# Kernel tuning notes

Measured on AMD Instinct MI355X. Metric: run time of the kernel, lower is better.

## Reference

```python
import jax, jax.numpy as jnp
import numpy as np

# --- dims (match init_kwargs) ---
B, T, S, K = 4, 128, 64, 2
CS = 1024            # codebook_size
NOTE_V, PHON_V = 128, 64
NE, PE, SE, PGB, PGE = 128, 128, 16, 8, 32
COND, TOK, PREV, D = 256, 256, 256, 512
NH, L_CTX, L_AUD = 8, 4, 6
HIST_WIN, AUD_WIN = 32, 64
DFF = 4 * D

CTX_KEYS = ["ln1_w","ln1_b","in_w","in_b","out_w","out_b","ln2_w","ln2_b","f1_w","f1_b","f2_w","f2_b"]


def _ln(x, w, b):
    m = x.mean(-1, keepdims=True)
    v = ((x - m) ** 2).mean(-1, keepdims=True)
    return (x - m) / jnp.sqrt(v + 1e-5) * w + b


def _mlp2(x, w1, b1, w2, b2, act):
    return act(x @ w1.T + b1) @ w2.T + b2


def _local_mask(n, win):
    i = jnp.arange(n)
    d = i[:, None] - i[None, :]
    return (d < 0) | (d >= win)   # True = masked (causal, local window)


def _mha(x, mask, in_w, in_b, out_w, out_b, nh):
    b, s, d = x.shape
    dh = d // nh
    q, k, v = jnp.split(x @ in_w.T + in_b, 3, axis=-1)
    sp = lambda t: t.reshape(b, s, nh, dh).transpose(0, 2, 1, 3)
    q, k, v = sp(q), sp(k), sp(v)
    sc = jnp.einsum('bhqd,bhkd->bhqk', q, k) * (1.0 / np.sqrt(dh))
    sc = jnp.where(mask, -1e9, sc)
    a = jax.nn.softmax(sc, axis=-1)
    o = jnp.einsum('bhqk,bhkd->bhqd', a, v).transpose(0, 2, 1, 3).reshape(b, s, d)
    return o @ out_w.T + out_b


def _block(x, mask, pr, nh):
    # pr: dict with ln1_w..f2_b for one layer (pre-norm attn + FFN, GELU)
    h = _ln(x, pr["ln1_w"], pr["ln1_b"])
    x = x + _mha(h, mask, pr["in_w"], pr["in_b"], pr["out_w"], pr["out_b"], nh)
    h2 = _ln(x, pr["ln2_w"], pr["ln2_b"])
    return x + _mlp2(h2, pr["f1_w"], pr["f1_b"], pr["f2_w"], pr["f2_b"],
                     lambda z: jax.nn.gelu(z, approximate=False))


def _forward(p, codes, note_id, phoneme_id, slur, phone_progress):
    silu = jax.nn.silu
    # ---- condition encoder ----
    cond_in = jnp.concatenate([
        p["note_emb_w"][note_id], p["phoneme_emb_w"][phoneme_id],
        p["slur_emb_w"][jnp.clip(slur, 0, 1)], p["pp_emb_w"][phone_progress]], -1)
    cond = _mlp2(cond_in, p["cond_w1"], p["cond_b1"], p["cond_w2"], p["cond_b2"], silu)
    # ---- shifted prev-step representation ----
    first = codes[..., 0]                       # [B,T,S]
    pooled = p["token_emb_w"][first].mean(2)    # [B,T,TOK]
    prev = _mlp2(pooled, p["prev_w1"], p["prev_b1"], p["prev_w2"], p["prev_b2"], silu)
    bos = jnp.broadcast_to(p["bos_step"], (B, 1, PREV))
    prev = jnp.concatenate([bos, prev[:, :-1]], 1)
    # ---- context transformer over steps (local causal window) ----
    h = _mlp2(jnp.concatenate([cond, prev], -1), p["step_w1"], p["step_b1"], p["step_w2"], p["step_b2"], silu)
    m_ctx = _local_mask(T, HIST_WIN)
    for l in range(L_CTX):
        pr = {k: p["ctx_" + k][l] for k in CTX_KEYS}
        h = _block(h, m_ctx, pr, NH)
    # ---- audio decoder over frames within each step ----
    tok = p["token_emb_w"][first] @ p["audio_in_w"].T + p["audio_in_b"]   # [B,T,S,D]
    bos_a = jnp.broadcast_to(p["audio_bos"], (B, T, 1, D))
    a = jnp.concatenate([bos_a, tok[:, :, :-1]], 2) + p["frame_pos"][None, None] + h[:, :, None]
    a = a.reshape(B * T, S, D)
    m_a = _local_mask(S, min(AUD_WIN, S))
    for l in range(L_AUD):
        pr = {k: p["aud_" + k][l] for k in CTX_KEYS}
        a = _block(a, m_a, pr, NH)
    ah = a.reshape(B, T, S, D)
    # ---- heads ----
    first_logits = (ah @ p["first_w"].T + p["first_b"])[..., None, :]     # [B,T,S,1,CS]
    rh = _mlp2(jnp.concatenate([ah, tok], -1), p["resc_w1"], p["resc_b1"], p["resc_w2"], p["resc_b2"], silu)
    res = jnp.einsum('btsd,kcd->btskc', rh, p["res_w"]) + p["res_b"]       # [B,T,S,K-1,CS]
    return jnp.concatenate([first_logits, res], axis=3)                    # [B,T,S,K,CS]


def setup_inputs() -> dict:
    key = jax.random.key(0)
    ks = iter(jax.random.split(key, 128))
    w = lambda *sh: jax.random.normal(next(ks), sh, jnp.float32) * 0.02
    z = lambda *sh: jnp.zeros(sh, jnp.float32)
    o = lambda *sh: jnp.ones(sh, jnp.float32)
    inp = {
        "codes": jax.random.randint(next(ks), (B, T, S, K), 0, CS, jnp.int32),
        "note_id": jax.random.randint(next(ks), (B, T), 0, NOTE_V, jnp.int32),
        "phoneme_id": jax.random.randint(next(ks), (B, T), 0, PHON_V, jnp.int32),
        "slur": jax.random.randint(next(ks), (B, T), 0, 2, jnp.int32),
        "phone_progress": jax.random.randint(next(ks), (B, T), 0, PGB, jnp.int32),
        "note_emb_w": w(NOTE_V, NE), "phoneme_emb_w": w(PHON_V, PE),
        "slur_emb_w": w(2, SE), "pp_emb_w": w(PGB, PGE),
        "cond_w1": w(COND, NE + PE + SE + PGE), "cond_b1": z(COND),
        "cond_w2": w(COND, COND), "cond_b2": z(COND),
        "token_emb_w": w(CS, TOK),
        "prev_w1": w(PREV, TOK), "prev_b1": z(PREV),
        "prev_w2": w(PREV, PREV), "prev_b2": z(PREV),
        "bos_step": z(PREV),
        "step_w1": w(D, COND + PREV), "step_b1": z(D),
        "step_w2": w(D, D), "step_b2": z(D),
        "audio_in_w": w(D, TOK), "audio_in_b": z(D),
        "audio_bos": z(D), "frame_pos": w(S, D),
        "first_w": w(CS, D), "first_b": z(CS),
        "resc_w1": w(D, 2 * D), "resc_b1": z(D),
        "resc_w2": w(D, D), "resc_b2": z(D),
        "res_w": w(K - 1, CS, D), "res_b": z(K - 1, CS),
    }
    for pre, L in (("ctx_", L_CTX), ("aud_", L_AUD)):
        inp[pre + "ln1_w"] = o(L, D); inp[pre + "ln1_b"] = z(L, D)
        inp[pre + "in_w"] = w(L, 3 * D, D); inp[pre + "in_b"] = z(L, 3 * D)
        inp[pre + "out_w"] = w(L, D, D); inp[pre + "out_b"] = z(L, D)
        inp[pre + "ln2_w"] = o(L, D); inp[pre + "ln2_b"] = z(L, D)
        inp[pre + "f1_w"] = w(L, DFF, D); inp[pre + "f1_b"] = z(L, DFF)
        inp[pre + "f2_w"] = w(L, D, DFF); inp[pre + "f2_b"] = z(L, D)
    return inp


FLOAT_KEYS = ["note_emb_w","phoneme_emb_w","slur_emb_w","pp_emb_w","cond_w1","cond_b1","cond_w2","cond_b2","token_emb_w","prev_w1","prev_b1","prev_w2","prev_b2","bos_step","step_w1","step_b1","step_w2","step_b2","audio_in_w","audio_in_b","audio_bos","frame_pos","first_w","first_b","resc_w1","resc_b1","resc_w2","resc_b2","res_w","res_b"] + [p + k for p in ("ctx_","aud_") for k in CTX_KEYS]


def reference(codes, note_id, phoneme_id, slur, phone_progress,
              note_emb_w, phoneme_emb_w, slur_emb_w, pp_emb_w,
              cond_w1, cond_b1, cond_w2, cond_b2, token_emb_w,
              prev_w1, prev_b1, prev_w2, prev_b2, bos_step,
              step_w1, step_b1, step_w2, step_b2,
              audio_in_w, audio_in_b, audio_bos, frame_pos,
              first_w, first_b, resc_w1, resc_b1, resc_w2, resc_b2, res_w, res_b,
              ctx_ln1_w, ctx_ln1_b, ctx_in_w, ctx_in_b, ctx_out_w, ctx_out_b,
              ctx_ln2_w, ctx_ln2_b, ctx_f1_w, ctx_f1_b, ctx_f2_w, ctx_f2_b,
              aud_ln1_w, aud_ln1_b, aud_in_w, aud_in_b, aud_out_w, aud_out_b,
              aud_ln2_w, aud_ln2_b, aud_f1_w, aud_f1_b, aud_f2_w, aud_f2_b):
    loc = locals()
    p = {k: loc[k] for k in FLOAT_KEYS}
    return _forward(p, codes, note_id, phoneme_id, slur, phone_progress)
```

## Files before the change

### kernel.cpp

```cpp
#include <hip/hip_runtime.h>
#include <cstdint>
#include <cstddef>

typedef unsigned short u16;
typedef short bf16x8 __attribute__((ext_vector_type(8)));
typedef float f32x4 __attribute__((ext_vector_type(4)));

__device__ __forceinline__ float bf2f(u16 u) { return __uint_as_float(((unsigned)u) << 16); }
__device__ __forceinline__ u16 f2bf(float f) {
  unsigned i = __float_as_uint(f);
  i += 0x7fffu + ((i >> 16) & 1u);
  return (u16)(i >> 16);
}
__device__ __forceinline__ unsigned packbf2(float lo, float hi) {
  return (unsigned)f2bf(lo) | ((unsigned)f2bf(hi) << 16);
}
__device__ __forceinline__ float lo16(unsigned u) { return __uint_as_float(u << 16); }
__device__ __forceinline__ float hi16(unsigned u) { return __uint_as_float(u & 0xffff0000u); }

__device__ __forceinline__ void async_ld16(u16* lds, const u16* g) {
  __builtin_amdgcn_global_load_lds((const __attribute__((address_space(1))) void*)g,
                                   (__attribute__((address_space(3))) void*)lds, 16, 0, 0);
}

__global__ void k_cast8(const float4* __restrict__ x, uint4* __restrict__ y, int n8) {
  int i = blockIdx.x * 256 + threadIdx.x;
  if (i >= n8) return;
  float4 a = x[(size_t)i * 2], b = x[(size_t)i * 2 + 1];
  uint4 o;
  o.x = packbf2(a.x, a.y); o.y = packbf2(a.z, a.w);
  o.z = packbf2(b.x, b.y); o.w = packbf2(b.z, b.w);
  y[i] = o;
}

template<int ACT, int OUTM>
__global__ __launch_bounds__(256)
void gemm_mfma(const u16* __restrict__ A, const u16* __restrict__ W,
               const float* __restrict__ bias, void* __restrict__ Cp,
               int M, int N, int K, int ldc) {
  __shared__ __align__(16) u16 SM[24576];
  const int tid = threadIdx.x;
  const int wave = tid >> 6, lane = tid & 63;

  const int gx = gridDim.x;
  const int nwg = gx * (int)gridDim.y;
  const int flat = (int)blockIdx.y * gx + (int)blockIdx.x;
  const int xcd = flat & 7, lo = flat >> 3;
  const int q = nwg >> 3, r = nwg & 7;
  const int swz = (xcd < r ? xcd * (q + 1) : r * (q + 1) + (xcd - r) * q) + lo;
  const int bm = (swz / gx) * 128, bn = (swz % gx) * 128;

  const int wm = (wave & 1) * 64, wn = (wave >> 1) * 64;
  const int srow = tid >> 2, selem = (tid & 3) * 8;
  const u16* Ap0 = A + (size_t)(bm + srow) * K + selem;
  const u16* Ap1 = A + (size_t)(bm + srow + 64) * K + selem;
  const u16* Wp0 = W + (size_t)(bn + srow) * K + selem;
  const u16* Wp1 = W + (size_t)(bn + srow + 64) * K + selem;
  const int fr = lane & 15, fq = (lane >> 4) * 8;

  f32x4 acc[4][4];
#pragma unroll
  for (int i = 0; i < 4; ++i)
#pragma unroll
    for (int j = 0; j < 4; ++j) acc[i][j] = (f32x4){0.f, 0.f, 0.f, 0.f};

  const int nt = K >> 5;

  auto stage = [&](int buf, int k0) {
    u16* AsD = SM + buf * 4096 + tid * 8;
    u16* BsD = SM + 12288 + buf * 4096 + tid * 8;
    async_ld16(AsD, Ap0 + k0);
    async_ld16(AsD + 2048, Ap1 + k0);
    async_ld16(BsD, Wp0 + k0);
    async_ld16(BsD + 2048, Wp1 + k0);
  };

  stage(0, 0);
  if (nt > 1) stage(1, 32);

  int bi = 0;
  for (int t = 0; t < nt; ++t) {
    if (t + 1 < nt) asm volatile("s_waitcnt vmcnt(4)" ::: "memory");
    else            asm volatile("s_waitcnt vmcnt(0)" ::: "memory");
    __builtin_amdgcn_s_barrier();
    if (t + 2 < nt) {
      int nb = bi + 2; if (nb >= 3) nb -= 3;
      stage(nb, (t + 2) << 5);
    }
    const u16* Asb = SM + bi * 4096;
    const u16* Bsb = SM + 12288 + bi * 4096;
    bf16x8 af[4], bfv[4];
#pragma unroll
    for (int i = 0; i < 4; ++i)
      af[i] = *(const bf16x8*)&Asb[(wm + i * 16 + fr) * 32 + fq];
#pragma unroll
    for (int j = 0; j < 4; ++j)
      bfv[j] = *(const bf16x8*)&Bsb[(wn + j * 16 + fr) * 32 + fq];
#pragma unroll
    for (int i = 0; i < 4; ++i)
#pragma unroll
      for (int j = 0; j < 4; ++j)
        acc[i][j] = __builtin_amdgcn_mfma_f32_16x16x32_bf16(af[i], bfv[j], acc[i][j], 0, 0, 0);
    if (++bi == 3) bi = 0;
  }

  __syncthreads();
  const int lrow = (lane >> 4) * 4;
  const int colb = wn + fr;

  if (OUTM == 0) {
    u16* Ep = SM;
#pragma unroll
    for (int j = 0; j < 4; ++j) {
      float bv = bias[bn + colb + j * 16];
#pragma unroll
      for (int i = 0; i < 4; ++i)
#pragma unroll
        for (int rr = 0; rr < 4; ++rr) {
          float v = acc[i][j][rr] + bv;
          if (ACT == 1) v = v / (1.f + __expf(-v));
          else if (ACT == 2) v = 0.5f * v * (1.f + erff(v * 0.70710678118f));
          Ep[(wm + i * 16 + lrow + rr) * 128 + colb + j * 16] = f2bf(v);
        }
    }
    __syncthreads();
#pragma unroll
    for (int it = 0; it < 8; ++it) {
      int idx = it * 256 + tid;
      int row = idx >> 4, c = idx & 15;
      *(uint4*)((u16*)Cp + (size_t)(bm + row) * ldc + bn + c * 8) =
          ((const uint4*)Ep)[idx];
    }
  } else {
    float* Ep = (float*)SM;
    float* Cf = (float*)Cp;
#pragma unroll
    for (int ch = 0; ch < 2; ++ch) {
      if ((wave & 1) == ch) {
#pragma unroll
        for (int j = 0; j < 4; ++j) {
          float bv = bias[bn + colb + j * 16];
#pragma unroll
          for (int i = 0; i < 4; ++i)
#pragma unroll
            for (int rr = 0; rr < 4; ++rr) {
              float v = acc[i][j][rr] + bv;
              if (ACT == 1) v = v / (1.f + __expf(-v));
              else if (ACT == 2) v = 0.5f * v * (1.f + erff(v * 0.70710678118f));
              Ep[(i * 16 + lrow + rr) * 128 + colb + j * 16] = v;
            }
        }
      }
      __syncthreads();
#pragma unroll
      for (int it = 0; it < 8; ++it) {
        int idx = it * 256 + tid;
        int row = idx >> 5, c4 = idx & 31;
        size_t g = (size_t)(bm + ch * 64 + row) * ldc + bn + c4 * 4;
        float4 sv = ((const float4*)Ep)[idx];
        if (OUTM == 1) {
          float4 od = *(const float4*)(Cf + g);
          sv.x += od.x; sv.y += od.y; sv.z += od.z; sv.w += od.w;
        }
        *(float4*)(Cf + g) = sv;
      }
      __syncthreads();
    }
  }
}

__global__ __launch_bounds__(256)
void k_layernorm(const float* __restrict__ X, const float* __restrict__ w,
                 const float* __restrict__ b, u16* __restrict__ Y) {
  int row = blockIdx.x, tid = threadIdx.x;
  const float* x = X + (size_t)row * 512;
  float v0 = x[tid], v1 = x[tid + 256];
  __shared__ float red[4];
  float s = v0 + v1;
  for (int o = 32; o; o >>= 1) s += __shfl_down(s, o, 64);
  if ((tid & 63) == 0) red[tid >> 6] = s;
  __syncthreads();
  if (tid == 0) red[0] = (red[0] + red[1] + red[2] + red[3]) * (1.f / 512.f);
  __syncthreads();
  float mean = red[0];
  __syncthreads();
  float d0 = v0 - mean, d1 = v1 - mean;
  float q = d0 * d0 + d1 * d1;
  for (int o = 32; o; o >>= 1) q += __shfl_down(q, o, 64);
  if ((tid & 63) == 0) red[tid >> 6] = q;
  __syncthreads();
  if (tid == 0) red[0] = (red[0] + red[1] + red[2] + red[3]) * (1.f / 512.f);
  __syncthreads();
  float rstd = rsqrtf(red[0] + 1e-5f);
  size_t o0 = (size_t)row * 512 + tid;
  Y[o0] = f2bf(d0 * rstd * w[tid] + b[tid]);
  Y[o0 + 256] = f2bf(d1 * rstd * w[tid + 256] + b[tid + 256]);
}

__global__ void k_cond_gather(const int* __restrict__ note_id, const int* __restrict__ phon_id,
                              const int* __restrict__ slur, const int* __restrict__ pp,
                              const float* __restrict__ note_emb, const float* __restrict__ phon_emb,
                              const float* __restrict__ slur_emb, const float* __restrict__ pp_emb,
                              u16* __restrict__ out) {
  int bt = blockIdx.x, t = threadIdx.x;
  u16 v = 0;
  if (t < 128) v = f2bf(note_emb[note_id[bt] * 128 + t]);
  else if (t < 256) v = f2bf(phon_emb[phon_id[bt] * 128 + (t - 128)]);
  else if (t < 272) {
    int sv = slur[bt]; sv = sv < 0 ? 0 : (sv > 1 ? 1 : sv);
    v = f2bf(slur_emb[sv * 16 + (t - 256)]);
  } else if (t < 304) v = f2bf(pp_emb[pp[bt] * 32 + (t - 272)]);
  out[bt * 320 + t] = v;
}

__global__ void k_pad_w(const float* __restrict__ w, u16* __restrict__ out) {
  int n = blockIdx.x, t = threadIdx.x;
  out[n * 320 + t] = (t < 304) ? f2bf(w[n * 304 + t]) : (u16)0;
}

__global__ void k_femb(const int* __restrict__ codes, const uint4* __restrict__ emb,
                       uint4* __restrict__ out) {
  int i = blockIdx.x * 256 + threadIdx.x;
  int m = i >> 5, c = i & 31;
  out[i] = emb[(size_t)codes[m * 2] * 32 + c];
}

__global__ void k_pool(const u16* __restrict__ femb, u16* __restrict__ pooled) {
  int bt = blockIdx.x, c = threadIdx.x;
  float s = 0.f;
  for (int j = 0; j < 64; ++j) s += bf2f(femb[((size_t)bt * 64 + j) * 256 + c]);
  pooled[bt * 256 + c] = f2bf(s * (1.f / 64.f));
}

__global__ void k_stepin(const u16* __restrict__ cond, const u16* __restrict__ prevo,
                         const float* __restrict__ bosf, u16* __restrict__ out) {
  int bt = blockIdx.x, t = threadIdx.x;
  u16 v;
  if (t < 256) v = cond[bt * 256 + t];
  else {
    int tt = bt & 127;
    v = (tt == 0) ? f2bf(bosf[t - 256]) : prevo[(bt - 1) * 256 + (t - 256)];
  }
  out[bt * 512 + t] = v;
}

__global__ __launch_bounds__(64)
void k_ctx_attn(const u16* __restrict__ qkv, u16* __restrict__ out) {
  int t = blockIdx.x, h = blockIdx.y, b = blockIdx.z;
  int lane = threadIdx.x;
  int bt = b * 128 + t;
  float qd = bf2f(qkv[(size_t)bt * 1536 + h * 64 + lane]) * 0.125f;
  int klo = t - 31; if (klo < 0) klo = 0;
  int n = t - klo + 1;
  __shared__ float sc[32];
  for (int i = 0; i < n; ++i) {
    float p = qd * bf2f(qkv[((size_t)(b * 128 + klo + i)) * 1536 + 512 + h * 64 + lane]);
    for (int o = 32; o; o >>= 1) p += __shfl_xor(p, o, 64);
    if (lane == 0) sc[i] = p;
  }
  __syncthreads();
  float mx = -1e30f;
  for (int i = 0; i < n; ++i) mx = fmaxf(mx, sc[i]);
  float den = 0.f, acc = 0.f;
  for (int i = 0; i < n; ++i) {
    float p = __expf(sc[i] - mx);
    den += p;
    acc += p * bf2f(qkv[((size_t)(b * 128 + klo + i)) * 1536 + 1024 + h * 64 + lane]);
  }
  out[(size_t)bt * 512 + h * 64 + lane] = f2bf(acc / den);
}

__global__ __launch_bounds__(128)
void k_aud_attn_mfma(const u16* __restrict__ qkv, u16* __restrict__ out) {
  constexpr int LP = 66;
  __shared__ u16 Pl[2][64 * LP];
  __shared__ u16 Vt[2][64 * LP];
  const int wave = threadIdx.x >> 6, lane = threadIdx.x & 63;
  const int id = blockIdx.x * 2 + wave;
  const int seq = id >> 3, h = id & 7;
  const u16* Qb = qkv + (size_t)seq * 64 * 1536 + h * 64;
  const u16* Kb = Qb + 512;
  const u16* Vb = Qb + 1024;
  u16* Plw = Pl[wave];
  u16* Vtw = Vt[wave];
  const int fr = lane & 15, fq = (lane >> 4) * 8;

#pragma unroll
  for (int t = 0; t < 8; ++t) {
    int vr = (lane >> 3) + 8 * t, vc = (lane & 7) * 8;
    uint4 vv = *(const uint4*)(Vb + (size_t)vr * 1536 + vc);
    Vtw[(vc + 0) * LP + vr] = (u16)(vv.x & 0xffff);
    Vtw[(vc + 1) * LP + vr] = (u16)(vv.x >> 16);
    Vtw[(vc + 2) * LP + vr] = (u16)(vv.y & 0xffff);
    Vtw[(vc + 3) * LP + vr] = (u16)(vv.y >> 16);
    Vtw[(vc + 4) * LP + vr] = (u16)(vv.z & 0xffff);
    Vtw[(vc + 5) * LP + vr] = (u16)(vv.z >> 16);
    Vtw[(vc + 6) * LP + vr] = (u16)(vv.w & 0xffff);
    Vtw[(vc + 7) * LP + vr] = (u16)(vv.w >> 16);
  }

  bf16x8 aq[4][2], bk[4][2];
#pragma unroll
  for (int i = 0; i < 4; ++i)
#pragma unroll
    for (int c = 0; c < 2; ++c) {
      aq[i][c] = *(const bf16x8*)(Qb + (size_t)(i * 16 + fr) * 1536 + fq + 32 * c);
      bk[i][c] = *(const bf16x8*)(Kb + (size_t)(i * 16 + fr) * 1536 + fq + 32 * c);
    }
  f32x4 s[4][4];
#pragma unroll
  for (int i = 0; i < 4; ++i)
#pragma unroll
    for (int j = 0; j < 4; ++j) s[i][j] = (f32x4){0.f, 0.f, 0.f, 0.f};
#pragma unroll
  for (int c = 0; c < 2; ++c)
#pragma unroll
    for (int i = 0; i < 4; ++i)
#pragma unroll
      for (int j = 0; j < 4; ++j)
        s[i][j] = __builtin_amdgcn_mfma_f32_16x16x32_bf16(aq[i][c], bk[j][c], s[i][j], 0, 0, 0);

  const int qr = (lane >> 4) * 4;
#pragma unroll
  for (int i = 0; i < 4; ++i) {
#pragma unroll
    for (int r = 0; r < 4; ++r) {
      int row = 16 * i + qr + r;
      float mx = -1e30f;
      float vj[4];
#pragma unroll
      for (int j = 0; j < 4; ++j) {
        float v = s[i][j][r] * 0.125f;
        if (16 * j + fr > row) v = -1e30f;
        vj[j] = v;
        mx = fmaxf(mx, v);
      }
      for (int o = 8; o; o >>= 1) mx = fmaxf(mx, __shfl_xor(mx, o, 64));
      float den = 0.f;
#pragma unroll
      for (int j = 0; j < 4; ++j) { vj[j] = __expf(vj[j] - mx); den += vj[j]; }
      for (int o = 8; o; o >>= 1) den += __shfl_xor(den, o, 64);
      float inv = 1.f / den;
#pragma unroll
      for (int j = 0; j < 4; ++j)
        Plw[row * LP + 16 * j + fr] = f2bf(vj[j] * inv);
    }
  }
  __syncthreads();

  f32x4 o4[4][4];
#pragma unroll
  for (int i = 0; i < 4; ++i)
#pragma unroll
    for (int j = 0; j < 4; ++j) o4[i][j] = (f32x4){0.f, 0.f, 0.f, 0.f};
#pragma unroll
  for (int c = 0; c < 2; ++c) {
    bf16x8 ap[4], bv[4];
#pragma unroll
    for (int i = 0; i < 4; ++i)
      ap[i] = *(const bf16x8*)&Plw[(16 * i + fr) * LP + fq + 32 * c];
#pragma unroll
    for (int j = 0; j < 4; ++j)
      bv[j] = *(const bf16x8*)&Vtw[(16 * j + fr) * LP + fq + 32 * c];
#pragma unroll
    for (int i = 0; i < 4; ++i)
#pragma unroll
      for (int j = 0; j < 4; ++j)
        o4[i][j] = __builtin_amdgcn_mfma_f32_16x16x32_bf16(ap[i], bv[j], o4[i][j], 0, 0, 0);
  }
#pragma unroll
  for (int i = 0; i < 4; ++i)
#pragma unroll
    for (int r = 0; r < 4; ++r) {
      int row = 16 * i + qr + r;
      u16* ob = out + ((size_t)seq * 64 + row) * 512 + h * 64;
#pragma unroll
      for (int j = 0; j < 4; ++j) ob[16 * j + fr] = f2bf(o4[i][j][r]);
    }
}

__global__ void k_abuild(const uint4* __restrict__ tok, const float4* __restrict__ bosf,
                         const float4* __restrict__ fpos, const float4* __restrict__ hstep,
                         float4* __restrict__ a) {
  size_t i = (size_t)blockIdx.x * 256 + threadIdx.x;
  int d8 = (int)(i & 63);
  size_t row = i >> 6;
  int s = (int)(row & 63);
  size_t bt = row >> 6;
  float t0, t1, t2, t3, t4, t5, t6, t7;
  if (s == 0) {
    float4 b0 = bosf[d8 * 2], b1 = bosf[d8 * 2 + 1];
    t0 = b0.x; t1 = b0.y; t2 = b0.z; t3 = b0.w;
    t4 = b1.x; t5 = b1.y; t6 = b1.z; t7 = b1.w;
  } else {
    uint4 tv = tok[(row - 1) * 64 + d8];
    t0 = lo16(tv.x); t1 = hi16(tv.x); t2 = lo16(tv.y); t3 = hi16(tv.y);
    t4 = lo16(tv.z); t5 = hi16(tv.z); t6 = lo16(tv.w); t7 = hi16(tv.w);
  }
  float4 f0 = fpos[(size_t)s * 128 + d8 * 2], f1 = fpos[(size_t)s * 128 + d8 * 2 + 1];
  float4 h0 = hstep[bt * 128 + d8 * 2], h1 = hstep[bt * 128 + d8 * 2 + 1];
  float4 o0, o1;
  o0.x = t0 + f0.x + h0.x; o0.y = t1 + f0.y + h0.y;
  o0.z = t2 + f0.z + h0.z; o0.w = t3 + f0.w + h0.w;
  o1.x = t4 + f1.x + h1.x; o1.y = t5 + f1.y + h1.y;
  o1.z = t6 + f1.z + h1.z; o1.w = t7 + f1.w + h1.w;
  a[i * 2] = o0; a[i * 2 + 1] = o1;
}

__global__ void k_cat(const uint4* __restrict__ ah, const uint4* __restrict__ tok,
                      uint4* __restrict__ out) {
  size_t i = (size_t)blockIdx.x * 256 + threadIdx.x;
  size_t m = i >> 7;
  int c = (int)(i & 127);
  out[i] = (c < 64) ? ah[m * 64 + c] : tok[m * 64 + (c - 64)];
}

template<int ACT, int OUTM>
static inline void gemm(const u16* A, const u16* W, const float* bias, void* C,
                        int M, int N, int K, int ldc, hipStream_t s) {
  gemm_mfma<ACT, OUTM><<<dim3(N / 128, M / 128), 256, 0, s>>>(A, W, bias, C, M, N, K, ldc);
}

static inline void cast_bf16(const float* x, u16* y, size_t n, hipStream_t s) {
  int n8 = (int)(n / 8);
  k_cast8<<<(n8 + 255) / 256, 256, 0, s>>>((const float4*)x, (uint4*)y, n8);
}

extern "C" void kernel_launch(void* const* d_in, const int* in_sizes, int n_in,
                              void* d_out, int out_size, void* d_ws, size_t ws_size,
                              hipStream_t stream) {
  const int* codes    = (const int*)d_in[0];
  const int* note_id  = (const int*)d_in[1];
  const int* phon_id  = (const int*)d_in[2];
  const int* slur     = (const int*)d_in[3];
  const int* pprog    = (const int*)d_in[4];
  const float* note_emb = (const float*)d_in[5];
  const float* phon_emb = (const float*)d_in[6];
  const float* slur_emb = (const float*)d_in[7];
  const float* pp_emb   = (const float*)d_in[8];
  const float* cond_w1  = (const float*)d_in[9];
  const float* cond_b1  = (const float*)d_in[10];
  const float* cond_w2  = (const float*)d_in[11];
  const float* cond_b2  = (const float*)d_in[12];
  const float* tok_emb  = (const float*)d_in[13];
  const float* prev_w1  = (const float*)d_in[14];
  const float* prev_b1  = (const float*)d_in[15];
  const float* prev_w2  = (const float*)d_in[16];
  const float* prev_b2  = (const float*)d_in[17];
  const float* bos_step = (const float*)d_in[18];
  const float* step_w1  = (const float*)d_in[19];
  const float* step_b1  = (const float*)d_in[20];
  const float* step_w2  = (const float*)d_in[21];
  const float* step_b2  = (const float*)d_in[22];
  const float* audio_in_w = (const float*)d_in[23];
  const float* audio_in_b = (const float*)d_in[24];
  const float* audio_bos  = (const float*)d_in[25];
  const float* frame_pos  = (const float*)d_in[26];
  const float* first_w  = (const float*)d_in[27];
  const float* first_b  = (const float*)d_in[28];
  const float* resc_w1  = (const float*)d_in[29];
  const float* resc_b1  = (const float*)d_in[30];
  const float* resc_w2  = (const float*)d_in[31];
  const float* resc_b2  = (const float*)d_in[32];
  const float* res_w    = (const float*)d_in[33];
  const float* res_b    = (const float*)d_in[34];
  const float* ctx_w[12]; for (int i = 0; i < 12; ++i) ctx_w[i] = (const float*)d_in[35 + i];
  const float* aud_w[12]; for (int i = 0; i < 12; ++i) aud_w[i] = (const float*)d_in[47 + i];

  char* p = (char*)d_ws;
  auto alloc = [&](size_t b) { char* r = p; p += (b + 255) & ~(size_t)255; return r; };
  float* A_res = (float*)alloc(32768ull * 512 * 4);
  u16* T_tok  = (u16*)alloc(32768ull * 512 * 2);
  u16* LNb    = (u16*)alloc(32768ull * 512 * 2);
  u16* AOb    = (u16*)alloc(32768ull * 512 * 2);
  u16* QF     = (u16*)alloc(32768ull * 2048 * 2);
  u16* f_emb  = (u16*)alloc(32768ull * 256 * 2);
  u16* temb   = (u16*)alloc(1024ull * 256 * 2);
  u16* cond_in = (u16*)alloc(512ull * 320 * 2);
  u16* cw1p   = (u16*)alloc(256ull * 320 * 2);
  u16* cw2    = (u16*)alloc(256ull * 256 * 2);
  u16* pw1    = (u16*)alloc(256ull * 256 * 2);
  u16* pw2    = (u16*)alloc(256ull * 256 * 2);
  u16* sw1    = (u16*)alloc(512ull * 512 * 2);
  u16* sw2    = (u16*)alloc(512ull * 512 * 2);
  u16* ainw   = (u16*)alloc(512ull * 256 * 2);
  u16* fw     = (u16*)alloc(1024ull * 512 * 2);
  u16* rw1    = (u16*)alloc(512ull * 1024 * 2);
  u16* rw2    = (u16*)alloc(512ull * 512 * 2);
  u16* resw   = (u16*)alloc(1024ull * 512 * 2);
  u16* cxin   = (u16*)alloc(4ull * 1536 * 512 * 2);
  u16* cxout  = (u16*)alloc(4ull * 512 * 512 * 2);
  u16* cxf1   = (u16*)alloc(4ull * 2048 * 512 * 2);
  u16* cxf2   = (u16*)alloc(4ull * 512 * 2048 * 2);
  u16* adin   = (u16*)alloc(6ull * 1536 * 512 * 2);
  u16* adout  = (u16*)alloc(6ull * 512 * 512 * 2);
  u16* adf1   = (u16*)alloc(6ull * 2048 * 512 * 2);
  u16* adf2   = (u16*)alloc(6ull * 512 * 2048 * 2);
  u16* cond_h = (u16*)alloc(512ull * 256 * 2);
  u16* condv  = (u16*)alloc(512ull * 256 * 2);
  u16* pooled = (u16*)alloc(512ull * 256 * 2);
  u16* prevh  = (u16*)alloc(512ull * 256 * 2);
  u16* prevo  = (u16*)alloc(512ull * 256 * 2);
  u16* stepin = (u16*)alloc(512ull * 512 * 2);
  u16* hmid   = (u16*)alloc(512ull * 512 * 2);
  float* hstep = (float*)alloc(512ull * 512 * 4);

  k_pad_w<<<256, 320, 0, stream>>>(cond_w1, cw1p);
  cast_bf16(cond_w2, cw2, 256ull * 256, stream);
  cast_bf16(prev_w1, pw1, 256ull * 256, stream);
  cast_bf16(prev_w2, pw2, 256ull * 256, stream);
  cast_bf16(step_w1, sw1, 512ull * 512, stream);
  cast_bf16(step_w2, sw2, 512ull * 512, stream);
  cast_bf16(tok_emb, temb, 1024ull * 256, stream);
  cast_bf16(audio_in_w, ainw, 512ull * 256, stream);
  cast_bf16(first_w, fw, 1024ull * 512, stream);
  cast_bf16(resc_w1, rw1, 512ull * 1024, stream);
  cast_bf16(resc_w2, rw2, 512ull * 512, stream);
  cast_bf16(res_w, resw, 1024ull * 512, stream);
  cast_bf16(ctx_w[2], cxin, 4ull * 1536 * 512, stream);
  cast_bf16(ctx_w[4], cxout, 4ull * 512 * 512, stream);
  cast_bf16(ctx_w[8], cxf1, 4ull * 2048 * 512, stream);
  cast_bf16(ctx_w[10], cxf2, 4ull * 512 * 2048, stream);
  cast_bf16(aud_w[2], adin, 6ull * 1536 * 512, stream);
  cast_bf16(aud_w[4], adout, 6ull * 512 * 512, stream);
  cast_bf16(aud_w[8], adf1, 6ull * 2048 * 512, stream);
  cast_bf16(aud_w[10], adf2, 6ull * 512 * 2048, stream);

  k_cond_gather<<<512, 320, 0, stream>>>(note_id, phon_id, slur, pprog,
                                         note_emb, phon_emb, slur_emb, pp_emb, cond_in);
  k_femb<<<4096, 256, 0, stream>>>(codes, (const uint4*)temb, (uint4*)f_emb);
  k_pool<<<512, 256, 0, stream>>>(f_emb, pooled);
  gemm<1, 0>(cond_in, cw1p, cond_b1, cond_h, 512, 256, 320, 256, stream);
  gemm<0, 0>(cond_h, cw2, cond_b2, condv, 512, 256, 256, 256, stream);
  gemm<1, 0>(pooled, pw1, prev_b1, prevh, 512, 256, 256, 256, stream);
  gemm<0, 0>(prevh, pw2, prev_b2, prevo, 512, 256, 256, 256, stream);
  k_stepin<<<512, 512, 0, stream>>>(condv, prevo, bos_step, stepin);
  gemm<1, 0>(stepin, sw1, step_b1, hmid, 512, 512, 512, 512, stream);
  gemm<0, 2>(hmid, sw2, step_b2, hstep, 512, 512, 512, 512, stream);

  for (int l = 0; l < 4; ++l) {
    k_layernorm<<<512, 256, 0, stream>>>(hstep, ctx_w[0] + l * 512, ctx_w[1] + l * 512, LNb);
    gemm<0, 0>(LNb, cxin + (size_t)l * 1536 * 512, ctx_w[3] + l * 1536, QF, 512, 1536, 512, 1536, stream);
    k_ctx_attn<<<dim3(128, 8, 4), 64, 0, stream>>>(QF, AOb);
    gemm<0, 1>(AOb, cxout + (size_t)l * 512 * 512, ctx_w[5] + l * 512, hstep, 512, 512, 512, 512, stream);
    k_layernorm<<<512, 256, 0, stream>>>(hstep, ctx_w[6] + l * 512, ctx_w[7] + l * 512, LNb);
    gemm<2, 0>(LNb, cxf1 + (size_t)l * 2048 * 512, ctx_w[9] + l * 2048, QF, 512, 2048, 512, 2048, stream);
    gemm<0, 1>(QF, cxf2 + (size_t)l * 512 * 2048, ctx_w[11] + l * 512, hstep, 512, 512, 2048, 512, stream);
  }

  gemm<0, 0>(f_emb, ainw, audio_in_b, T_tok, 32768, 512, 256, 512, stream);
  k_abuild<<<8192, 256, 0, stream>>>((const uint4*)T_tok, (const float4*)audio_bos,
                                     (const float4*)frame_pos, (const float4*)hstep, (float4*)A_res);
  for (int l = 0; l < 6; ++l) {
    k_layernorm<<<32768, 256, 0, stream>>>(A_res, aud_w[0] + l * 512, aud_w[1] + l * 512, LNb);
    gemm<0, 0>(LNb, adin + (size_t)l * 1536 * 512, aud_w[3] + l * 1536, QF, 32768, 1536, 512, 1536, stream);
    k_aud_attn_mfma<<<2048, 128, 0, stream>>>(QF, AOb);
    gemm<0, 1>(AOb, adout + (size_t)l * 512 * 512, aud_w[5] + l * 512, A_res, 32768, 512, 512, 512, stream);
    k_layernorm<<<32768, 256, 0, stream>>>(A_res, aud_w[6] + l * 512, aud_w[7] + l * 512, LNb);
    gemm<2, 0>(LNb, adf1 + (size_t)l * 2048 * 512, aud_w[9] + l * 2048, QF, 32768, 2048, 512, 2048, stream);
    gemm<0, 1>(QF, adf2 + (size_t)l * 512 * 2048, aud_w[11] + l * 512, A_res, 32768, 512, 2048, 512, stream);
  }

  {
    int n8 = 32768 * 512 / 8;
    k_cast8<<<(n8 + 255) / 256, 256, 0, stream>>>((const float4*)A_res, (uint4*)LNb, n8);
  }
  gemm<0, 2>(LNb, fw, first_b, (float*)d_out, 32768, 1024, 512, 2048, stream);
  k_cat<<<16384, 256, 0, stream>>>((const uint4*)LNb, (const uint4*)T_tok, (uint4*)QF);
  gemm<1, 0>(QF, rw1, resc_b1, AOb, 32768, 512, 1024, 512, stream);
  gemm<0, 0>(AOb, rw2, resc_b2, T_tok, 32768, 512, 512, 512, stream);
  gemm<0, 2>(T_tok, resw, res_b, (float*)d_out + 1024, 32768, 1024, 512, 2048, stream);
}
```

Before: 3.622 ms.

## Add 256x256-tile MFMA GEMM with XCD swizzle for large audio GEMMs

Adds a new 512-thread GEMM kernel that computes 256x256 output tiles per workgroup. It double-buffers 64-wide K slices through LDS with async global-to-LDS loads and splits each K step into four MFMA phases separated by barriers, with raised wave priority around the MFMAs. Workgroups are remapped across XCDs. All large M=32768 GEMMs now use it, which raises operand reuse and cuts global traffic per FLOP. The cost is 128KB of LDS per block, more registers and lower occupancy, plus a dependency on N being divisible by 256.

```diff
diff --git a/kernel.cpp b/kernel.cpp
--- a/kernel.cpp
+++ b/kernel.cpp
@@ -21,6 +21,12 @@
 __device__ __forceinline__ void async_ld16(u16* lds, const u16* g) {
   __builtin_amdgcn_global_load_lds((const __attribute__((address_space(1))) void*)g,
                                    (__attribute__((address_space(3))) void*)lds, 16, 0, 0);
+}
+
+__device__ __forceinline__ void fbar() {
+  __builtin_amdgcn_sched_barrier(0);
+  __builtin_amdgcn_s_barrier();
+  __builtin_amdgcn_sched_barrier(0);
 }
 
 __global__ void k_cast8(const float4* __restrict__ x, uint4* __restrict__ y, int n8) {
@@ -157,6 +163,193 @@
         int idx = it * 256 + tid;
         int row = idx >> 5, c4 = idx & 31;
         size_t g = (size_t)(bm + ch * 64 + row) * ldc + bn + c4 * 4;
+        float4 sv = ((const float4*)Ep)[idx];
+        if (OUTM == 1) {
+          float4 od = *(const float4*)(Cf + g);
+          sv.x += od.x; sv.y += od.y; sv.z += od.z; sv.w += od.w;
+        }
+        *(float4*)(Cf + g) = sv;
+      }
+      __syncthreads();
+    }
+  }
+}
+
+template<int ACT, int OUTM>
+__global__ __launch_bounds__(512, 2)
+void gemm_mfma256(const u16* __restrict__ A, const u16* __restrict__ W,
+                  const float* __restrict__ bias, void* __restrict__ Cp,
+                  int M, int N, int K, int ldc) {
+  __shared__ __align__(16) u16 SM[65536];
+  const int tid = threadIdx.x;
+  const int wave = tid >> 6, lane = tid & 63;
+  const int wave_m = wave >> 2, wave_n = wave & 3;
+  const int WM = wave_m * 128, WN = wave_n * 64;
+
+  const int gx = gridDim.x;
+  const int nwg = gx * (int)gridDim.y;
+  const int flat = (int)blockIdx.y * gx + (int)blockIdx.x;
+  const int xcd = flat & 7, lo = flat >> 3;
+  const int q = nwg >> 3, r = nwg & 7;
+  const int swz = (xcd < r ? xcd * (q + 1) : r * (q + 1) + (xcd - r) * q) + lo;
+  const int bm = (swz / gx) * 256, bn = (swz % gx) * 256;
+
+  const int srow = tid >> 3;
+  const int slc = (tid & 7) ^ (srow & 7);
+  const u16* Asrc = A + (size_t)(bm + srow) * K + slc * 8;
+  const u16* Wsrc = W + (size_t)(bn + srow) * K + slc * 8;
+
+  auto stage = [&](int buf, int k0) {
+    u16* Ad = SM + buf * 32768 + tid * 8;
+    u16* Bd = SM + buf * 32768 + 16384 + tid * 8;
+#pragma unroll
+    for (int qq = 0; qq < 4; ++qq)
+      async_ld16(Ad + qq * 4096, Asrc + (size_t)qq * 64 * K + k0);
+#pragma unroll
+    for (int qq = 0; qq < 4; ++qq)
+      async_ld16(Bd + qq * 4096, Wsrc + (size_t)qq * 64 * K + k0);
+  };
+
+  const int fr = lane & 15;
+  const int pc0 = (((lane >> 4) ^ (fr & 7))) * 8;
+  const int arow0 = (WM + fr) * 64;
+  const int brow0 = (WN + fr) * 64;
+
+  f32x4 acc[8][4];
+#pragma unroll
+  for (int i = 0; i < 8; ++i)
+#pragma unroll
+    for (int j = 0; j < 4; ++j) acc[i][j] = (f32x4){0.f, 0.f, 0.f, 0.f};
+
+  const int nt = K >> 6;
+
+  stage(0, 0);
+  if (nt > 1) stage(1, 64);
+
+  bf16x8 aA[4][2], bB[4][2];
+
+#pragma unroll 1
+  for (int t = 0; t < nt; ++t) {
+    const u16* Ab = SM + (t & 1) * 32768;
+    const u16* Bb = Ab + 16384;
+    if (t + 1 < nt) asm volatile("s_waitcnt vmcnt(8)" ::: "memory");
+    else            asm volatile("s_waitcnt vmcnt(0)" ::: "memory");
+    fbar();
+#pragma unroll
+    for (int mi = 0; mi < 4; ++mi)
+#pragma unroll
+      for (int ks = 0; ks < 2; ++ks)
+        aA[mi][ks] = *(const bf16x8*)&Ab[arow0 + mi * 1024 + (pc0 ^ (ks * 32))];
+#pragma unroll
+    for (int nj = 0; nj < 2; ++nj)
+#pragma unroll
+      for (int ks = 0; ks < 2; ++ks)
+        bB[nj][ks] = *(const bf16x8*)&Bb[brow0 + nj * 1024 + (pc0 ^ (ks * 32))];
+    __builtin_amdgcn_s_setprio(1);
+#pragma unroll
+    for (int mi = 0; mi < 4; ++mi)
+#pragma unroll
+      for (int nj = 0; nj < 2; ++nj)
+#pragma unroll
+        for (int ks = 0; ks < 2; ++ks)
+          acc[mi][nj] = __builtin_amdgcn_mfma_f32_16x16x32_bf16(aA[mi][ks], bB[nj][ks], acc[mi][nj], 0, 0, 0);
+    __builtin_amdgcn_s_setprio(0);
+    fbar();
+#pragma unroll
+    for (int nj = 2; nj < 4; ++nj)
+#pragma unroll
+      for (int ks = 0; ks < 2; ++ks)
+        bB[nj][ks] = *(const bf16x8*)&Bb[brow0 + nj * 1024 + (pc0 ^ (ks * 32))];
+    __builtin_amdgcn_s_setprio(1);
+#pragma unroll
+    for (int mi = 0; mi < 4; ++mi)
+#pragma unroll
+      for (int nj = 2; nj < 4; ++nj)
+#pragma unroll
+        for (int ks = 0; ks < 2; ++ks)
+          acc[mi][nj] = __builtin_amdgcn_mfma_f32_16x16x32_bf16(aA[mi][ks], bB[nj][ks], acc[mi][nj], 0, 0, 0);
+    __builtin_amdgcn_s_setprio(0);
+    fbar();
+#pragma unroll
+    for (int mi = 0; mi < 4; ++mi)
+#pragma unroll
+      for (int ks = 0; ks < 2; ++ks)
+        aA[mi][ks] = *(const bf16x8*)&Ab[arow0 + (mi + 4) * 1024 + (pc0 ^ (ks * 32))];
+    __builtin_amdgcn_s_setprio(1);
+#pragma unroll
+    for (int mi = 0; mi < 4; ++mi)
+#pragma unroll
+      for (int nj = 2; nj < 4; ++nj)
+#pragma unroll
+        for (int ks = 0; ks < 2; ++ks)
+          acc[mi + 4][nj] = __builtin_amdgcn_mfma_f32_16x16x32_bf16(aA[mi][ks], bB[nj][ks], acc[mi + 4][nj], 0, 0, 0);
+    __builtin_amdgcn_s_setprio(0);
+    fbar();
+    if (t + 2 < nt) stage(t & 1, (t + 2) << 6);
+    __builtin_amdgcn_s_setprio(1);
+#pragma unroll
+    for (int mi = 0; mi < 4; ++mi)
+#pragma unroll
+      for (int nj = 0; nj < 2; ++nj)
+#pragma unroll
+        for (int ks = 0; ks < 2; ++ks)
+          acc[mi + 4][nj] = __builtin_amdgcn_mfma_f32_16x16x32_bf16(aA[mi][ks], bB[nj][ks], acc[mi + 4][nj], 0, 0, 0);
+    __builtin_amdgcn_s_setprio(0);
+  }
+
+  fbar();
+  const int lrow = (lane >> 4) * 4;
+  const int colb = WN + fr;
+
+  if (OUTM == 0) {
+    u16* Ep = SM;
+#pragma unroll
+    for (int nj = 0; nj < 4; ++nj) {
+      float bv = bias[bn + colb + nj * 16];
+#pragma unroll
+      for (int mi = 0; mi < 8; ++mi)
+#pragma unroll
+        for (int rr = 0; rr < 4; ++rr) {
+          float v = acc[mi][nj][rr] + bv;
+          if (ACT == 1) v = v / (1.f + __expf(-v));
+          else if (ACT == 2) v = 0.5f * v * (1.f + erff(v * 0.70710678118f));
+          Ep[(WM + mi * 16 + lrow + rr) * 256 + colb + nj * 16] = f2bf(v);
+        }
+    }
+    __syncthreads();
+#pragma unroll
+    for (int it = 0; it < 16; ++it) {
+      int idx = it * 512 + tid;
+      int row = idx >> 5, c = idx & 31;
+      *(uint4*)((u16*)Cp + (size_t)(bm + row) * ldc + bn + c * 8) =
+          ((const uint4*)Ep)[idx];
+    }
+  } else {
+    float* Ep = (float*)SM;
+    float* Cf = (float*)Cp;
+#pragma unroll
+    for (int ch = 0; ch < 2; ++ch) {
+      if (wave_m == ch) {
+#pragma unroll
+        for (int nj = 0; nj < 4; ++nj) {
+          float bv = bias[bn + colb + nj * 16];
+#pragma unroll
+          for (int mi = 0; mi < 8; ++mi)
+#pragma unroll
+            for (int rr = 0; rr < 4; ++rr) {
+              float v = acc[mi][nj][rr] + bv;
+              if (ACT == 1) v = v / (1.f + __expf(-v));
+              else if (ACT == 2) v = 0.5f * v * (1.f + erff(v * 0.70710678118f));
+              Ep[(mi * 16 + lrow + rr) * 256 + colb + nj * 16] = v;
+            }
+        }
+      }
+      __syncthreads();
+#pragma unroll
+      for (int it = 0; it < 16; ++it) {
+        int idx = it * 512 + tid;
+        int row = idx >> 6, c4 = idx & 63;
+        size_t g = (size_t)(bm + ch * 128 + row) * ldc + bn + c4 * 4;
         float4 sv = ((const float4*)Ep)[idx];
         if (OUTM == 1) {
           float4 od = *(const float4*)(Cf + g);
@@ -419,6 +612,12 @@
 static inline void gemm(const u16* A, const u16* W, const float* bias, void* C,
                         int M, int N, int K, int ldc, hipStream_t s) {
   gemm_mfma<ACT, OUTM><<<dim3(N / 128, M / 128), 256, 0, s>>>(A, W, bias, C, M, N, K, ldc);
+}
+
+template<int ACT, int OUTM>
+static inline void gemmBig(const u16* A, const u16* W, const float* bias, void* C,
+                           int M, int N, int K, int ldc, hipStream_t s) {
+  gemm_mfma256<ACT, OUTM><<<dim3(N / 256, M / 256), 512, 0, s>>>(A, W, bias, C, M, N, K, ldc);
 }
 
 static inline void cast_bf16(const float* x, u16* y, size_t n, hipStream_t s) {
@@ -548,26 +747,26 @@
     gemm<0, 1>(QF, cxf2 + (size_t)l * 512 * 2048, ctx_w[11] + l * 512, hstep, 512, 512, 2048, 512, stream);
   }
 
-  gemm<0, 0>(f_emb, ainw, audio_in_b, T_tok, 32768, 512, 256, 512, stream);
+  gemmBig<0, 0>(f_emb, ainw, audio_in_b, T_tok, 32768, 512, 256, 512, stream);
   k_abuild<<<8192, 256, 0, stream>>>((const uint4*)T_tok, (const float4*)audio_bos,
                                      (const float4*)frame_pos, (const float4*)hstep, (float4*)A_res);
   for (int l = 0; l < 6; ++l) {
     k_layernorm<<<32768, 256, 0, stream>>>(A_res, aud_w[0] + l * 512, aud_w[1] + l * 512, LNb);
-    gemm<0, 0>(LNb, adin + (size_t)l * 1536 * 512, aud_w[3] + l * 1536, QF, 32768, 1536, 512, 1536, stream);
+    gemmBig<0, 0>(LNb, adin + (size_t)l * 1536 * 512, aud_w[3] + l * 1536, QF, 32768, 1536, 512, 1536, stream);
     k_aud_attn_mfma<<<2048, 128, 0, stream>>>(QF, AOb);
-    gemm<0, 1>(AOb, adout + (size_t)l * 512 * 512, aud_w[5] + l * 512, A_res, 32768, 512, 512, 512, stream);
+    gemmBig<0, 1>(AOb, adout + (size_t)l * 512 * 512, aud_w[5] + l * 512, A_res, 32768, 512, 512, 512, stream);
     k_layernorm<<<32768, 256, 0, stream>>>(A_res, aud_w[6] + l * 512, aud_w[7] + l * 512, LNb);
-    gemm<2, 0>(LNb, adf1 + (size_t)l * 2048 * 512, aud_w[9] + l * 2048, QF, 32768, 2048, 512, 2048, stream);
-    gemm<0, 1>(QF, adf2 + (size_t)l * 512 * 2048, aud_w[11] + l * 512, A_res, 32768, 512, 2048, 512, stream);
+    gemmBig<2, 0>(LNb, adf1 + (size_t)l * 2048 * 512, aud_w[9] + l * 2048, QF, 32768, 2048, 512, 2048, stream);
+    gemmBig<0, 1>(QF, adf2 + (size_t)l * 512 * 2048, aud_w[11] + l * 512, A_res, 32768, 512, 2048, 512, stream);
   }
 
   {
     int n8 = 32768 * 512 / 8;
     k_cast8<<<(n8 + 255) / 256, 256, 0, stream>>>((const float4*)A_res, (uint4*)LNb, n8);
   }
-  gemm<0, 2>(LNb, fw, first_b, (float*)d_out, 32768, 1024, 512, 2048, stream);
+  gemmBig<0, 2>(LNb, fw, first_b, (float*)d_out, 32768, 1024, 512, 2048, stream);
   k_cat<<<16384, 256, 0, stream>>>((const uint4*)LNb, (const uint4*)T_tok, (uint4*)QF);
-  gemm<1, 0>(QF, rw1, resc_b1, AOb, 32768, 512, 1024, 512, stream);
-  gemm<0, 0>(AOb, rw2, resc_b2, T_tok, 32768, 512, 512, 512, stream);
-  gemm<0, 2>(T_tok, resw, res_b, (float*)d_out + 1024, 32768, 1024, 512, 2048, stream);
-}
+  gemmBig<1, 0>(QF, rw1, resc_b1, AOb, 32768, 512, 1024, 512, stream);
+  gemmBig<0, 0>(AOb, rw2, resc_b2, T_tok, 32768, 512, 512, 512, stream);
+  gemmBig<0, 2>(T_tok, resw, res_b, (float*)d_out + 1024, 32768, 1024, 512, 2048, stream);
+}
```

New measurement: 3.601 ms. No clear change (-0.6%).
